# Optimization experiments

Hardware: AMD Instinct MI355X
Metric: run time of the kernel (lower is better)

The kernel has to match this reference:

```python
import jax, jax.numpy as jnp
import numpy as np

N, CIN, T, V, COUT = 64, 64, 256, 25, 128
CI = COUT // 2  # inter_channels
EPS = 1e-5


def setup_inputs() -> dict:
    key = jax.random.key(0)
    ks = jax.random.split(key, 12)
    s = 0.05
    d = {}
    d['x'] = jax.random.normal(ks[0], (N, CIN, T, V), jnp.float32)
    d['A'] = jax.random.normal(ks[1], (3, V, V), jnp.float32) * s
    d['Al'] = jax.random.normal(ks[2], (3, V, V), jnp.float32) * s
    d['Wp'] = jax.random.normal(ks[3], (3, COUT, CIN), jnp.float32) * s
    d['bp'] = jnp.zeros((3, COUT), jnp.float32)
    d['Wm1'] = jax.random.normal(ks[4], (CI, CIN), jnp.float32) * s
    d['bm1'] = jnp.zeros((CI,), jnp.float32)
    d['Wm2'] = jax.random.normal(ks[5], (CI, CIN), jnp.float32) * s
    d['bm2'] = jnp.zeros((CI,), jnp.float32)
    d['Wm3'] = jax.random.normal(ks[6], (COUT, CI), jnp.float32) * s
    d['bm3'] = jnp.zeros((COUT,), jnp.float32)
    d['Wm4'] = jax.random.normal(ks[7], (COUT, CIN), jnp.float32) * s
    d['bm4'] = jnp.zeros((COUT,), jnp.float32)
    d['alpha'] = jax.random.normal(ks[8], (1,), jnp.float32) * s
    d['bn_gamma'] = jnp.ones((COUT,), jnp.float32)
    d['bn_beta'] = jnp.zeros((COUT,), jnp.float32)
    d['down_W'] = jax.random.normal(ks[9], (COUT, CIN), jnp.float32) * s
    d['down_gamma'] = jnp.ones((COUT,), jnp.float32)
    d['down_beta'] = jnp.zeros((COUT,), jnp.float32)
    return d


def _bn_train(y, gamma, beta):
    # BatchNorm2d training forward: biased batch stats over (N, T, V)
    mu = jnp.mean(y, axis=(0, 2, 3), keepdims=True)
    var = jnp.var(y, axis=(0, 2, 3), keepdims=True)
    return (y - mu) * jax.lax.rsqrt(var + EPS) * gamma[None, :, None, None] + beta[None, :, None, None]


def reference(x, A, Al, Wp, bp, Wm1, bm1, Wm2, bm2, Wm3, bm3, Wm4, bm4,
              alpha, bn_gamma, bn_beta, down_W, down_gamma, down_beta):
    Tn = x.shape[2]
    # --- static graph branch: sum over 3 subsets of (A+Al) graph matmuls ---
    Xp = jnp.einsum('soi,nitv->snotv', Wp, x) + bp[:, None, :, None, None]  # (3,N,COUT,T,V)
    y = jnp.einsum('suv,snctv->nctu', A + Al, Xp)                           # (N,COUT,T,V)
    # --- dynamic adjacency from temporal-difference features ---
    xf = jnp.mean(jnp.einsum('oi,nitv->notv', Wm1, x[:, :, :Tn - 2]) + bm1[None, :, None, None], axis=2)  # (N,CI,V)
    xb = jnp.mean(jnp.einsum('oi,nitv->notv', Wm2, x[:, :, 2:]) + bm2[None, :, None, None], axis=2)       # (N,CI,V)
    diff = xb[:, :, :, None] - xf[:, :, None, :]                            # (N,CI,V,V)
    Rd = jnp.tanh(jnp.einsum('oi,nivw->novw', Wm3, diff) + bm3[None, :, None, None])  # (N,COUT,V,V)
    Xm = jnp.einsum('oi,nitv->notv', Wm4, x) + bm4[None, :, None, None]     # (N,COUT,T,V)
    z = jnp.einsum('ncuv,nctv->nctu', Rd, Xm)                               # (N,COUT,T,V)
    y = z * alpha + y
    # --- BN, residual (1x1 conv + BN down-path since CIN != COUT), ReLU ---
    y = _bn_train(y, bn_gamma, bn_beta)
    d = jnp.einsum('oi,nitv->notv', down_W, x)  # no bias
    d = _bn_train(d, down_gamma, down_beta)
    return jax.nn.relu(y + d)
```

## Files before the change

### kernel.cpp

```cpp
#include <hip/hip_runtime.h>
#include <stdint.h>

typedef unsigned short u16;
typedef unsigned int   u32;
typedef short bf16x8 __attribute__((ext_vector_type(8)));
typedef float f32x4  __attribute__((ext_vector_type(4)));

#define N_    64
#define CIN_  64
#define T_    256
#define V_    25
#define COUT_ 128
#define CI_   64
#define EPS_  1e-5f
#define CNT_  409600.0f

#define MFMA16(a,b,c) __builtin_amdgcn_mfma_f32_16x16x32_bf16((a),(b),(c),0,0,0)

__device__ __forceinline__ u16 f2bf(float f) {
  u32 u = __float_as_uint(f);
  u += 0x7fffu + ((u >> 16) & 1u);
  return (u16)(u >> 16);
}
__device__ __forceinline__ float bf2f(u16 h) { return __uint_as_float(((u32)h) << 16); }

__global__ __launch_bounds__(256) void k_pack(const float* __restrict__ Wp, const float* __restrict__ Wm4,
                                              const float* __restrict__ dW, const float* __restrict__ A,
                                              const float* __restrict__ Al,
                                              u16* __restrict__ w5, u16* __restrict__ bst) {
  int tid = threadIdx.x;
  for (int i = tid; i < 640 * 64; i += 256) {
    int r = i >> 6, k = i & 63;
    float v = (r < 384) ? Wp[i] : (r < 512) ? Wm4[(r - 384) * 64 + k] : dW[(r - 512) * 64 + k];
    w5[i] = f2bf(v);
  }
  for (int i = tid; i < 3 * 32 * 32; i += 256) {
    int s = i >> 10, rem = i & 1023, u = rem >> 5, v = rem & 31;
    float val = (u < 25 && v < 25) ? (A[(s * 25 + u) * 25 + v] + Al[(s * 25 + u) * 25 + v]) : 0.f;
    bst[i] = f2bf(val);
  }
}

__global__ __launch_bounds__(256) void k_means(const float* __restrict__ x,
                                               float* __restrict__ mf, float* __restrict__ mb) {
  int i = blockIdx.x, n = blockIdx.y;
  const float* src = x + ((size_t)n * CIN_ + i) * T_ * V_;
  __shared__ float xs[T_ * V_];
  __shared__ float pf[8][32], pb[8][32];
  for (int idx = threadIdx.x; idx < T_ * V_; idx += 256) xs[idx] = src[idx];
  __syncthreads();
  int v = threadIdx.x & 31, g = threadIdx.x >> 5;
  float sf = 0.f, sb = 0.f;
  if (v < V_) {
    for (int t = g; t < T_; t += 8) {
      float val = xs[t * V_ + v];
      if (t < T_ - 2) sf += val;
      if (t >= 2)     sb += val;
    }
  }
  pf[g][v] = sf; pb[g][v] = sb;
  __syncthreads();
  if (threadIdx.x < V_) {
    float af = 0.f, ab = 0.f;
    for (int gg = 0; gg < 8; gg++) { af += pf[gg][threadIdx.x]; ab += pb[gg][threadIdx.x]; }
    size_t o = ((size_t)n * CIN_ + i) * V_ + threadIdx.x;
    mf[o] = af * (1.0f / 254.0f);
    mb[o] = ab * (1.0f / 254.0f);
  }
}

__global__ __launch_bounds__(256) void k_rd(
    const float* __restrict__ mf, const float* __restrict__ mb,
    const float* __restrict__ Wm1, const float* __restrict__ bm1,
    const float* __restrict__ Wm2, const float* __restrict__ bm2,
    const float* __restrict__ Wm3, const float* __restrict__ bm3,
    const float* __restrict__ bm4, const float* __restrict__ alpha,
    const float* __restrict__ A, const float* __restrict__ Al, const float* __restrict__ bp,
    u16* __restrict__ rdws, float* __restrict__ biasws) {
  int n = blockIdx.x;
  int tid = threadIdx.x;
  __shared__ float MfL[CIN_][V_], MbL[CIN_][V_], xfL[CI_][V_], xbL[CI_][V_];
  __shared__ float PL[COUT_ * V_], QL[COUT_ * V_], rsumL[3][V_];
  for (int idx = tid; idx < CIN_ * V_; idx += 256) {
    MfL[idx / V_][idx % V_] = mf[(size_t)n * CIN_ * V_ + idx];
    MbL[idx / V_][idx % V_] = mb[(size_t)n * CIN_ * V_ + idx];
  }
  if (tid < 75) {
    int s = tid / 25, u = tid % 25;
    float acc = 0.f;
    for (int v = 0; v < 25; v++) acc += A[(s * 25 + u) * 25 + v] + Al[(s * 25 + u) * 25 + v];
    rsumL[s][u] = acc;
  }
  __syncthreads();
  for (int idx = tid; idx < CI_ * V_; idx += 256) {
    int o = idx / V_, v = idx % V_;
    float af = bm1[o], ab = bm2[o];
    for (int i = 0; i < CIN_; i++) {
      af += Wm1[o * CIN_ + i] * MfL[i][v];
      ab += Wm2[o * CIN_ + i] * MbL[i][v];
    }
    xfL[o][v] = af; xbL[o][v] = ab;
  }
  __syncthreads();
  for (int idx = tid; idx < COUT_ * V_; idx += 256) {
    int c = idx / V_, u = idx % V_;
    float p = 0.f, q = 0.f;
    for (int i = 0; i < CI_; i++) {
      p += Wm3[c * CI_ + i] * xbL[i][u];
      q += Wm3[c * CI_ + i] * xfL[i][u];
    }
    PL[idx] = p; QL[idx] = q;
  }
  __syncthreads();
  float al = alpha[0];
  for (int r = tid; r < COUT_ * V_; r += 256) {
    int c = r / V_, u = r % V_;
    float pv = PL[r] + bm3[c];
    float acc = 0.f;
    u16* dst = rdws + ((size_t)(n * COUT_ + c) * 25 + u) * 32;
    for (int w = 0; w < 25; w++) {
      float val = al * tanhf(pv - QL[c * V_ + w]);
      dst[w] = f2bf(val);
      acc += val;
    }
    for (int w = 25; w < 32; w++) dst[w] = 0;
    float yb = 0.f;
    for (int s = 0; s < 3; s++) yb += bp[s * COUT_ + c] * rsumL[s][u];
    biasws[(size_t)(n * COUT_ + c) * 25 + u] = bm4[c] * acc + yb;
  }
}

__global__ __launch_bounds__(256, 2) void k_main(
    const float* __restrict__ x, const u16* __restrict__ w5, const u16* __restrict__ bst,
    const u16* __restrict__ rdws, const float* __restrict__ biasws,
    u16* __restrict__ out16, float* __restrict__ partials) {
  __shared__ __align__(16) char smem[59904];
  __shared__ float statsL[512];
  const int tid = threadIdx.x;
  const int w = tid >> 6, l = tid & 63;
  const int lc = l & 15, lq = l >> 4;
  const int n = blockIdx.y, tc = blockIdx.x, t0 = tc * 16;

  {
    u32* xslw = (u32*)smem;
    const float* xb = x + (size_t)n * CIN_ * T_ * V_ + (size_t)t0 * V_;
    for (int idx = tid; idx < 32 * 416; idx += 256) {
      int i2 = idx / 416, p = idx - i2 * 416;
      float a = 0.f, b = 0.f;
      if (p < 400) {
        a = xb[(size_t)(2 * i2)     * (T_ * V_) + p];
        b = xb[(size_t)(2 * i2 + 1) * (T_ * V_) + p];
      }
      xslw[p * 36 + i2] = ((u32)f2bf(b) << 16) | (u32)f2bf(a);
    }
  }
  bf16x8 bw[3][2];
  #pragma unroll
  for (int s = 0; s < 3; s++)
    #pragma unroll
    for (int ut = 0; ut < 2; ut++)
      bw[s][ut] = *(const bf16x8*)(bst + (s * 32 + ut * 16 + lc) * 32 + lq * 8);
  __syncthreads();

  bf16x8 xf[7][2] = {};
  #pragma unroll
  for (int pi = 0; pi < 7; pi++) {
    int pt = w + pi * 4;
    if (pt < 26) {
      #pragma unroll
      for (int ks = 0; ks < 2; ks++)
        xf[pi][ks] = *(const bf16x8*)((const u16*)smem + (pt * 16 + lc) * 72 + ks * 32 + lq * 8);
    }
  }
  __syncthreads();

  {
    uint4 z4 = {0, 0, 0, 0};
    uint4* q = (uint4*)smem;
    for (int idx = tid; idx < 2304; idx += 256) q[idx] = z4;
    statsL[tid] = 0.f; statsL[tid + 256] = 0.f;
  }
  __syncthreads();

  u16* xpl = (u16*)smem;
  const f32x4 zz = {0.f, 0.f, 0.f, 0.f};

  for (int g = 0; g < 8; g++) {
    const int c0 = g * 16;
    f32x4 acc[4][2];
    #pragma unroll
    for (int cl = 0; cl < 4; cl++) { acc[cl][0] = zz; acc[cl][1] = zz; }
    float ds[4] = {0.f, 0.f, 0.f, 0.f}, dq[4] = {0.f, 0.f, 0.f, 0.f};

    #pragma unroll
    for (int h = 0; h < 2; h++) {
      const int nsl = h ? 3 : 2;
      bf16x8 af[3][2];
      #pragma unroll
      for (int si = 0; si < 3; si++) if (si < nsl) {
        int sl = h * 2 + si;
        #pragma unroll
        for (int ks = 0; ks < 2; ks++)
          af[si][ks] = *(const bf16x8*)(w5 + ((sl * 128 + c0 + lc) * 64 + ks * 32 + lq * 8));
      }
      #pragma unroll
      for (int pi = 0; pi < 7; pi++) {
        int pt = w + pi * 4;
        if (pt >= 26) continue;
        f32x4 pa[3];
        #pragma unroll
        for (int si = 0; si < 3; si++) if (si < nsl) {
          pa[si] = MFMA16(af[si][0], xf[pi][0], zz);
          pa[si] = MFMA16(af[si][1], xf[pi][1], pa[si]);
        }
        int p = pt * 16 + lc;
        if (p < 400) {
          u32 up = (u32)p, t = up / 25u, v = up - t * 25u;
          #pragma unroll
          for (int si = 0; si < 3; si++) if (si < nsl) {
            int sl = h * 2 + si;
            if (sl < 4) {
              int slot = sl & 1;
              u16* dst = xpl + (4 * lq) * 1152 + t * 72 + slot * 32 + v;
              #pragma unroll
              for (int r = 0; r < 4; r++) dst[r * 1152] = f2bf(pa[si][r]);
            } else {
              size_t ob = (((size_t)(n * COUT_ + c0 + 4 * lq) * T_ + t0 + t) * V_ + v) * 2 + 1;
              #pragma unroll
              for (int r = 0; r < 4; r++) {
                float dv = pa[si][r];
                out16[ob + (size_t)r * (T_ * V_ * 2)] = f2bf(dv);
                ds[r] += dv; dq[r] += dv * dv;
              }
            }
          }
        }
      }
      if (h == 1) {
        #pragma unroll
        for (int r = 0; r < 4; r++) {
          float a = ds[r], b = dq[r];
          #pragma unroll
          for (int off = 1; off < 16; off <<= 1) { a += __shfl_xor(a, off); b += __shfl_xor(b, off); }
          if (lc == 0) {
            atomicAdd(&statsL[(c0 + 4 * lq + r) * 4 + 2], a);
            atomicAdd(&statsL[(c0 + 4 * lq + r) * 4 + 3], b);
          }
        }
      }
      __syncthreads();

      {
        bf16x8 rdf0[4], rdf1[4];
        if (h == 1) {
          #pragma unroll
          for (int cl = 0; cl < 4; cl++) {
            size_t rb = (size_t)(n * COUT_ + c0 + w * 4 + cl) * 25;
            rdf0[cl] = *(const bf16x8*)(rdws + (rb + lc) * 32 + lq * 8);
            int u1c = (lc + 16 < 25) ? lc + 16 : 24;
            rdf1[cl] = *(const bf16x8*)(rdws + (rb + u1c) * 32 + lq * 8);
          }
        }
        #pragma unroll
        for (int cl = 0; cl < 4; cl++) {
          int clocal = w * 4 + cl;
          #pragma unroll
          for (int kl = 0; kl < 2; kl++) {
            bf16x8 aX = *(const bf16x8*)(xpl + clocal * 1152 + lc * 72 + kl * 32 + lq * 8);
            int kk = h * 2 + kl;
            bf16x8 b0, b1;
            if (kk < 3) { b0 = bw[kk][0]; b1 = bw[kk][1]; }
            else        { b0 = rdf0[cl];  b1 = rdf1[cl]; }
            acc[cl][0] = MFMA16(aX, b0, acc[cl][0]);
            acc[cl][1] = MFMA16(aX, b1, acc[cl][1]);
          }
        }
      }
      if (h == 1) {
        #pragma unroll
        for (int cl = 0; cl < 4; cl++) {
          int c = c0 + w * 4 + cl;
          size_t bb = (size_t)(n * COUT_ + c) * 25;
          float bias0 = biasws[bb + lc];
          int u1 = lc + 16; bool v1 = u1 < 25;
          float bias1 = biasws[bb + (v1 ? u1 : 24)];
          size_t ob = ((size_t)(n * COUT_ + c) * T_ + t0) * V_;
          float sy = 0.f, sq = 0.f;
          #pragma unroll
          for (int r = 0; r < 4; r++) {
            int t = 4 * lq + r;
            float y0 = acc[cl][0][r] + bias0;
            out16[(ob + t * 25 + lc) * 2] = f2bf(y0);
            sy += y0; sq += y0 * y0;
            float y1 = acc[cl][1][r] + bias1;
            if (v1) {
              out16[(ob + t * 25 + u1) * 2] = f2bf(y1);
              sy += y1; sq += y1 * y1;
            }
          }
          #pragma unroll
          for (int off = 1; off < 64; off <<= 1) { sy += __shfl_xor(sy, off); sq += __shfl_xor(sq, off); }
          if (l == 0) { atomicAdd(&statsL[c * 4 + 0], sy); atomicAdd(&statsL[c * 4 + 1], sq); }
        }
      }
      __syncthreads();
    }
  }
  int bflat = blockIdx.y * 16 + blockIdx.x;
  for (int j = tid; j < 512; j += 256) partials[(size_t)j * 1024 + bflat] = statsL[j];
}

__global__ __launch_bounds__(256) void k_stats1(const float* __restrict__ partials, float* __restrict__ colsum) {
  int w = threadIdx.x >> 6, l = threadIdx.x & 63;
  for (int ci = 0; ci < 8; ci++) {
    int j = blockIdx.x * 32 + w * 8 + ci;
    float s = 0.f;
    for (int it = 0; it < 16; it++) s += partials[(size_t)j * 1024 + it * 64 + l];
    #pragma unroll
    for (int off = 1; off < 64; off <<= 1) s += __shfl_xor(s, off);
    if (l == 0) colsum[j] = s;
  }
}

__global__ __launch_bounds__(128) void k_stats2(
    const float* __restrict__ colsum,
    const float* __restrict__ bn_g, const float* __restrict__ bn_b,
    const float* __restrict__ dn_g, const float* __restrict__ dn_b,
    float* __restrict__ params) {
  int c = threadIdx.x;
  float sy = colsum[c * 4], syy = colsum[c * 4 + 1], sd = colsum[c * 4 + 2], sdd = colsum[c * 4 + 3];
  float muY = sy / CNT_, varY = syy / CNT_ - muY * muY;
  float muD = sd / CNT_, varD = sdd / CNT_ - muD * muD;
  float sY = bn_g[c] * rsqrtf(varY + EPS_);
  float sD = dn_g[c] * rsqrtf(varD + EPS_);
  float off = bn_b[c] - muY * sY + dn_b[c] - muD * sD;
  params[c * 4 + 0] = sY; params[c * 4 + 1] = sD; params[c * 4 + 2] = off;
}

__global__ __launch_bounds__(256) void k_final(u32* __restrict__ io, const float* __restrict__ params) {
  int slab = blockIdx.x;
  int c = slab & (COUT_ - 1);
  float sY = params[c * 4], sD = params[c * 4 + 1], off = params[c * 4 + 2];
  size_t base = (size_t)slab * (T_ * V_);
  #pragma unroll 5
  for (int j = 0; j < 25; j++) {
    size_t idx = base + j * 256 + threadIdx.x;
    u32 w = io[idx];
    float y = bf2f((u16)(w & 0xffffu));
    float d = bf2f((u16)(w >> 16));
    float val = fmaf(y, sY, fmaf(d, sD, off));
    io[idx] = __float_as_uint(fmaxf(val, 0.0f));
  }
}

extern "C" void kernel_launch(void* const* d_in, const int* in_sizes, int n_in,
                              void* d_out, int out_size, void* d_ws, size_t ws_size,
                              hipStream_t stream) {
  const float* x    = (const float*)d_in[0];
  const float* A    = (const float*)d_in[1];
  const float* Al   = (const float*)d_in[2];
  const float* Wp   = (const float*)d_in[3];
  const float* bp   = (const float*)d_in[4];
  const float* Wm1  = (const float*)d_in[5];
  const float* bm1  = (const float*)d_in[6];
  const float* Wm2  = (const float*)d_in[7];
  const float* bm2  = (const float*)d_in[8];
  const float* Wm3  = (const float*)d_in[9];
  const float* bm3  = (const float*)d_in[10];
  const float* Wm4  = (const float*)d_in[11];
  const float* bm4  = (const float*)d_in[12];
  const float* alpha= (const float*)d_in[13];
  const float* bn_g = (const float*)d_in[14];
  const float* bn_b = (const float*)d_in[15];
  const float* dW   = (const float*)d_in[16];
  const float* dn_g = (const float*)d_in[17];
  const float* dn_b = (const float*)d_in[18];

  char* ws = (char*)d_ws;
  float* mf       = (float*)(ws + 0);
  float* mb       = (float*)(ws + 409600);
  u16*   rdws     = (u16*)  (ws + 819200);
  float* biasws   = (float*)(ws + 13926400);
  u16*   w5       = (u16*)  (ws + 14745600);
  u16*   bstw     = (u16*)  (ws + 14827520);
  float* partials = (float*)(ws + 14833664);
  float* colsum   = (float*)(ws + 16930816);
  float* params   = (float*)(ws + 16932864);

  k_pack <<<dim3(1),       dim3(256), 0, stream>>>(Wp, Wm4, dW, A, Al, w5, bstw);
  k_means<<<dim3(64, 64),  dim3(256), 0, stream>>>(x, mf, mb);
  k_rd   <<<dim3(64),      dim3(256), 0, stream>>>(mf, mb, Wm1, bm1, Wm2, bm2, Wm3, bm3,
                                                   bm4, alpha, A, Al, bp, rdws, biasws);
  k_main <<<dim3(16, 64),  dim3(256), 0, stream>>>(x, w5, bstw, rdws, biasws,
                                                   (u16*)d_out, partials);
  k_stats1<<<dim3(16),     dim3(256), 0, stream>>>(partials, colsum);
  k_stats2<<<dim3(1),      dim3(128), 0, stream>>>(colsum, bn_g, bn_b, dn_g, dn_b, params);
  k_final<<<dim3(64 * 128),dim3(256), 0, stream>>>((u32*)d_out, params);
}
```

Baseline: 679.5 us.

## Shrink k_main LDS for 3 blocks/CU, stage down-path in LDS, vectorize final pass

k_main now stages x in two 32-channel halves, which cuts shared memory so the launch bounds can ask for three blocks per CU instead of two. The down-path conv output is buffered in LDS and written with y as one packed 32-bit store, replacing scattered 16-bit global stores. Its statistics are reduced in the same epilogue pass as y. Separately, k_pack and k_stats1 get wider grids and k_final uses 128-bit loads and stores. The risk is register pressure under the tighter occupancy target and the extra LDS traffic and barriers.

```diff
diff --git a/kernel.cpp b/kernel.cpp
--- a/kernel.cpp
+++ b/kernel.cpp
@@ -28,13 +28,13 @@
                                               const float* __restrict__ dW, const float* __restrict__ A,
                                               const float* __restrict__ Al,
                                               u16* __restrict__ w5, u16* __restrict__ bst) {
-  int tid = threadIdx.x;
-  for (int i = tid; i < 640 * 64; i += 256) {
+  int tid0 = blockIdx.x * 256 + threadIdx.x, stride = gridDim.x * 256;
+  for (int i = tid0; i < 640 * 64; i += stride) {
     int r = i >> 6, k = i & 63;
     float v = (r < 384) ? Wp[i] : (r < 512) ? Wm4[(r - 384) * 64 + k] : dW[(r - 512) * 64 + k];
     w5[i] = f2bf(v);
   }
-  for (int i = tid; i < 3 * 32 * 32; i += 256) {
+  for (int i = tid0; i < 3 * 32 * 32; i += stride) {
     int s = i >> 10, rem = i & 1023, u = rem >> 5, v = rem & 31;
     float val = (u < 25 && v < 25) ? (A[(s * 25 + u) * 25 + v] + Al[(s * 25 + u) * 25 + v]) : 0.f;
     bst[i] = f2bf(val);
@@ -130,29 +130,37 @@
   }
 }
 
-__global__ __launch_bounds__(256, 2) void k_main(
+__global__ __launch_bounds__(256, 3) void k_main(
     const float* __restrict__ x, const u16* __restrict__ w5, const u16* __restrict__ bst,
     const u16* __restrict__ rdws, const float* __restrict__ biasws,
-    u16* __restrict__ out16, float* __restrict__ partials) {
-  __shared__ __align__(16) char smem[59904];
+    u32* __restrict__ out32, float* __restrict__ partials) {
+  __shared__ __align__(16) char smem[36864];
+  __shared__ u16 dls[16 * 425];
   __shared__ float statsL[512];
   const int tid = threadIdx.x;
   const int w = tid >> 6, l = tid & 63;
   const int lc = l & 15, lq = l >> 4;
   const int n = blockIdx.y, tc = blockIdx.x, t0 = tc * 16;
 
-  {
+  bf16x8 xf[7][2] = {};
+  const float* xb = x + (size_t)n * CIN_ * T_ * V_ + (size_t)t0 * V_;
+  #pragma unroll
+  for (int hf = 0; hf < 2; hf++) {
     u32* xslw = (u32*)smem;
-    const float* xb = x + (size_t)n * CIN_ * T_ * V_ + (size_t)t0 * V_;
-    for (int idx = tid; idx < 32 * 416; idx += 256) {
-      int i2 = idx / 416, p = idx - i2 * 416;
-      float a = 0.f, b = 0.f;
-      if (p < 400) {
-        a = xb[(size_t)(2 * i2)     * (T_ * V_) + p];
-        b = xb[(size_t)(2 * i2 + 1) * (T_ * V_) + p];
-      }
-      xslw[p * 36 + i2] = ((u32)f2bf(b) << 16) | (u32)f2bf(a);
-    }
+    for (int idx = tid; idx < 16 * 400; idx += 256) {
+      int i2 = idx / 400, p = idx - i2 * 400;
+      float a = xb[(size_t)(hf * 32 + 2 * i2)     * (T_ * V_) + p];
+      float b = xb[(size_t)(hf * 32 + 2 * i2 + 1) * (T_ * V_) + p];
+      xslw[p * 18 + i2] = ((u32)f2bf(b) << 16) | (u32)f2bf(a);
+    }
+    __syncthreads();
+    #pragma unroll
+    for (int pi = 0; pi < 7; pi++) {
+      int pt = w + pi * 4;
+      if (pt < 25)
+        xf[pi][hf] = *(const bf16x8*)((const u16*)smem + (pt * 16 + lc) * 36 + lq * 8);
+    }
+    __syncthreads();
   }
   bf16x8 bw[3][2];
   #pragma unroll
@@ -160,19 +168,6 @@
     #pragma unroll
     for (int ut = 0; ut < 2; ut++)
       bw[s][ut] = *(const bf16x8*)(bst + (s * 32 + ut * 16 + lc) * 32 + lq * 8);
-  __syncthreads();
-
-  bf16x8 xf[7][2] = {};
-  #pragma unroll
-  for (int pi = 0; pi < 7; pi++) {
-    int pt = w + pi * 4;
-    if (pt < 26) {
-      #pragma unroll
-      for (int ks = 0; ks < 2; ks++)
-        xf[pi][ks] = *(const bf16x8*)((const u16*)smem + (pt * 16 + lc) * 72 + ks * 32 + lq * 8);
-    }
-  }
-  __syncthreads();
 
   {
     uint4 z4 = {0, 0, 0, 0};
@@ -190,7 +185,6 @@
     f32x4 acc[4][2];
     #pragma unroll
     for (int cl = 0; cl < 4; cl++) { acc[cl][0] = zz; acc[cl][1] = zz; }
-    float ds[4] = {0.f, 0.f, 0.f, 0.f}, dq[4] = {0.f, 0.f, 0.f, 0.f};
 
     #pragma unroll
     for (int h = 0; h < 2; h++) {
@@ -206,101 +200,88 @@
       #pragma unroll
       for (int pi = 0; pi < 7; pi++) {
         int pt = w + pi * 4;
-        if (pt >= 26) continue;
+        if (pt >= 25) continue;
         f32x4 pa[3];
         #pragma unroll
         for (int si = 0; si < 3; si++) if (si < nsl) {
           pa[si] = MFMA16(af[si][0], xf[pi][0], zz);
           pa[si] = MFMA16(af[si][1], xf[pi][1], pa[si]);
         }
-        int p = pt * 16 + lc;
-        if (p < 400) {
-          u32 up = (u32)p, t = up / 25u, v = up - t * 25u;
-          #pragma unroll
-          for (int si = 0; si < 3; si++) if (si < nsl) {
-            int sl = h * 2 + si;
-            if (sl < 4) {
-              int slot = sl & 1;
-              u16* dst = xpl + (4 * lq) * 1152 + t * 72 + slot * 32 + v;
-              #pragma unroll
-              for (int r = 0; r < 4; r++) dst[r * 1152] = f2bf(pa[si][r]);
-            } else {
-              size_t ob = (((size_t)(n * COUT_ + c0 + 4 * lq) * T_ + t0 + t) * V_ + v) * 2 + 1;
-              #pragma unroll
-              for (int r = 0; r < 4; r++) {
-                float dv = pa[si][r];
-                out16[ob + (size_t)r * (T_ * V_ * 2)] = f2bf(dv);
-                ds[r] += dv; dq[r] += dv * dv;
-              }
-            }
+        u32 up = (u32)(pt * 16 + lc), t = up / 25u, v = up - t * 25u;
+        #pragma unroll
+        for (int si = 0; si < 3; si++) if (si < nsl) {
+          int sl = h * 2 + si;
+          if (sl < 4) {
+            int slot = sl & 1;
+            u16* dst = xpl + (4 * lq) * 1152 + t * 72 + slot * 32 + v;
+            #pragma unroll
+            for (int r = 0; r < 4; r++) dst[r * 1152] = f2bf(pa[si][r]);
+          } else {
+            u16* dst = dls + (4 * lq) * 425 + t * 26 + v;
+            #pragma unroll
+            for (int r = 0; r < 4; r++) dst[r * 425] = f2bf(pa[si][r]);
           }
         }
       }
+      __syncthreads();
+
+      bf16x8 rdf0[4], rdf1[4];
       if (h == 1) {
         #pragma unroll
-        for (int r = 0; r < 4; r++) {
-          float a = ds[r], b = dq[r];
-          #pragma unroll
-          for (int off = 1; off < 16; off <<= 1) { a += __shfl_xor(a, off); b += __shfl_xor(b, off); }
-          if (lc == 0) {
-            atomicAdd(&statsL[(c0 + 4 * lq + r) * 4 + 2], a);
-            atomicAdd(&statsL[(c0 + 4 * lq + r) * 4 + 3], b);
-          }
-        }
-      }
-      __syncthreads();
-
-      {
-        bf16x8 rdf0[4], rdf1[4];
-        if (h == 1) {
-          #pragma unroll
-          for (int cl = 0; cl < 4; cl++) {
-            size_t rb = (size_t)(n * COUT_ + c0 + w * 4 + cl) * 25;
-            rdf0[cl] = *(const bf16x8*)(rdws + (rb + lc) * 32 + lq * 8);
-            int u1c = (lc + 16 < 25) ? lc + 16 : 24;
-            rdf1[cl] = *(const bf16x8*)(rdws + (rb + u1c) * 32 + lq * 8);
-          }
-        }
-        #pragma unroll
         for (int cl = 0; cl < 4; cl++) {
-          int clocal = w * 4 + cl;
-          #pragma unroll
-          for (int kl = 0; kl < 2; kl++) {
-            bf16x8 aX = *(const bf16x8*)(xpl + clocal * 1152 + lc * 72 + kl * 32 + lq * 8);
-            int kk = h * 2 + kl;
-            bf16x8 b0, b1;
-            if (kk < 3) { b0 = bw[kk][0]; b1 = bw[kk][1]; }
-            else        { b0 = rdf0[cl];  b1 = rdf1[cl]; }
-            acc[cl][0] = MFMA16(aX, b0, acc[cl][0]);
-            acc[cl][1] = MFMA16(aX, b1, acc[cl][1]);
-          }
+          size_t rb = (size_t)(n * COUT_ + c0 + w * 4 + cl) * 25;
+          rdf0[cl] = *(const bf16x8*)(rdws + (rb + lc) * 32 + lq * 8);
+          int u1c = (lc + 16 < 25) ? lc + 16 : 24;
+          rdf1[cl] = *(const bf16x8*)(rdws + (rb + u1c) * 32 + lq * 8);
+        }
+      }
+      #pragma unroll
+      for (int cl = 0; cl < 4; cl++) {
+        int clocal = w * 4 + cl;
+        #pragma unroll
+        for (int kl = 0; kl < 2; kl++) {
+          bf16x8 aX = *(const bf16x8*)(xpl + clocal * 1152 + lc * 72 + kl * 32 + lq * 8);
+          int kk = h * 2 + kl;
+          bf16x8 b0, b1;
+          if (kk < 3) { b0 = bw[kk][0]; b1 = bw[kk][1]; }
+          else        { b0 = rdf0[cl];  b1 = rdf1[cl]; }
+          acc[cl][0] = MFMA16(aX, b0, acc[cl][0]);
+          acc[cl][1] = MFMA16(aX, b1, acc[cl][1]);
         }
       }
       if (h == 1) {
         #pragma unroll
         for (int cl = 0; cl < 4; cl++) {
-          int c = c0 + w * 4 + cl;
+          int cloc = w * 4 + cl, c = c0 + cloc;
           size_t bb = (size_t)(n * COUT_ + c) * 25;
           float bias0 = biasws[bb + lc];
           int u1 = lc + 16; bool v1 = u1 < 25;
           float bias1 = biasws[bb + (v1 ? u1 : 24)];
           size_t ob = ((size_t)(n * COUT_ + c) * T_ + t0) * V_;
-          float sy = 0.f, sq = 0.f;
+          float sy = 0.f, sq = 0.f, sd = 0.f, sdq = 0.f;
           #pragma unroll
           for (int r = 0; r < 4; r++) {
             int t = 4 * lq + r;
             float y0 = acc[cl][0][r] + bias0;
-            out16[(ob + t * 25 + lc) * 2] = f2bf(y0);
-            sy += y0; sq += y0 * y0;
-            float y1 = acc[cl][1][r] + bias1;
+            float d0 = bf2f(dls[cloc * 425 + t * 26 + lc]);
+            out32[ob + t * 25 + lc] = ((u32)f2bf(d0) << 16) | (u32)f2bf(y0);
+            sy += y0; sq += y0 * y0; sd += d0; sdq += d0 * d0;
             if (v1) {
-              out16[(ob + t * 25 + u1) * 2] = f2bf(y1);
-              sy += y1; sq += y1 * y1;
+              float y1 = acc[cl][1][r] + bias1;
+              float d1 = bf2f(dls[cloc * 425 + t * 26 + u1]);
+              out32[ob + t * 25 + u1] = ((u32)f2bf(d1) << 16) | (u32)f2bf(y1);
+              sy += y1; sq += y1 * y1; sd += d1; sdq += d1 * d1;
             }
           }
           #pragma unroll
-          for (int off = 1; off < 64; off <<= 1) { sy += __shfl_xor(sy, off); sq += __shfl_xor(sq, off); }
-          if (l == 0) { atomicAdd(&statsL[c * 4 + 0], sy); atomicAdd(&statsL[c * 4 + 1], sq); }
+          for (int off = 1; off < 64; off <<= 1) {
+            sy += __shfl_xor(sy, off); sq += __shfl_xor(sq, off);
+            sd += __shfl_xor(sd, off); sdq += __shfl_xor(sdq, off);
+          }
+          if (l == 0) {
+            atomicAdd(&statsL[c * 4 + 0], sy);  atomicAdd(&statsL[c * 4 + 1], sq);
+            atomicAdd(&statsL[c * 4 + 2], sd);  atomicAdd(&statsL[c * 4 + 3], sdq);
+          }
         }
       }
       __syncthreads();
@@ -311,15 +292,16 @@
 }
 
 __global__ __launch_bounds__(256) void k_stats1(const float* __restrict__ partials, float* __restrict__ colsum) {
-  int w = threadIdx.x >> 6, l = threadIdx.x & 63;
-  for (int ci = 0; ci < 8; ci++) {
-    int j = blockIdx.x * 32 + w * 8 + ci;
-    float s = 0.f;
-    for (int it = 0; it < 16; it++) s += partials[(size_t)j * 1024 + it * 64 + l];
-    #pragma unroll
-    for (int off = 1; off < 64; off <<= 1) s += __shfl_xor(s, off);
-    if (l == 0) colsum[j] = s;
-  }
+  __shared__ float red[4];
+  int j = blockIdx.x, tid = threadIdx.x;
+  float s = 0.f;
+  #pragma unroll
+  for (int i = 0; i < 4; i++) s += partials[(size_t)j * 1024 + i * 256 + tid];
+  #pragma unroll
+  for (int off = 1; off < 64; off <<= 1) s += __shfl_xor(s, off);
+  if ((tid & 63) == 0) red[tid >> 6] = s;
+  __syncthreads();
+  if (tid == 0) colsum[j] = red[0] + red[1] + red[2] + red[3];
 }
 
 __global__ __launch_bounds__(128) void k_stats2(
@@ -337,19 +319,26 @@
   params[c * 4 + 0] = sY; params[c * 4 + 1] = sD; params[c * 4 + 2] = off;
 }
 
-__global__ __launch_bounds__(256) void k_final(u32* __restrict__ io, const float* __restrict__ params) {
+__global__ __launch_bounds__(256) void k_final(uint4* __restrict__ io, const float* __restrict__ params) {
   int slab = blockIdx.x;
   int c = slab & (COUT_ - 1);
   float sY = params[c * 4], sD = params[c * 4 + 1], off = params[c * 4 + 2];
-  size_t base = (size_t)slab * (T_ * V_);
-  #pragma unroll 5
-  for (int j = 0; j < 25; j++) {
-    size_t idx = base + j * 256 + threadIdx.x;
-    u32 w = io[idx];
-    float y = bf2f((u16)(w & 0xffffu));
-    float d = bf2f((u16)(w >> 16));
-    float val = fmaf(y, sY, fmaf(d, sD, off));
-    io[idx] = __float_as_uint(fmaxf(val, 0.0f));
+  size_t base = (size_t)slab * 1600;
+  #pragma unroll
+  for (int j = 0; j < 7; j++) {
+    int idx = j * 256 + threadIdx.x;
+    if (idx < 1600) {
+      uint4 wv = io[base + idx];
+      u32 ws[4] = {wv.x, wv.y, wv.z, wv.w};
+      #pragma unroll
+      for (int e = 0; e < 4; e++) {
+        float y = bf2f((u16)(ws[e] & 0xffffu));
+        float d = bf2f((u16)(ws[e] >> 16));
+        float val = fmaf(y, sY, fmaf(d, sD, off));
+        ws[e] = __float_as_uint(fmaxf(val, 0.0f));
+      }
+      io[base + idx] = make_uint4(ws[0], ws[1], ws[2], ws[3]);
+    }
   }
 }
 
@@ -387,13 +376,13 @@
   float* colsum   = (float*)(ws + 16930816);
   float* params   = (float*)(ws + 16932864);
 
-  k_pack <<<dim3(1),       dim3(256), 0, stream>>>(Wp, Wm4, dW, A, Al, w5, bstw);
+  k_pack <<<dim3(41),      dim3(256), 0, stream>>>(Wp, Wm4, dW, A, Al, w5, bstw);
   k_means<<<dim3(64, 64),  dim3(256), 0, stream>>>(x, mf, mb);
   k_rd   <<<dim3(64),      dim3(256), 0, stream>>>(mf, mb, Wm1, bm1, Wm2, bm2, Wm3, bm3,
                                                    bm4, alpha, A, Al, bp, rdws, biasws);
   k_main <<<dim3(16, 64),  dim3(256), 0, stream>>>(x, w5, bstw, rdws, biasws,
-                                                   (u16*)d_out, partials);
-  k_stats1<<<dim3(16),     dim3(256), 0, stream>>>(partials, colsum);
+                                                   (u32*)d_out, partials);
+  k_stats1<<<dim3(512),    dim3(256), 0, stream>>>(partials, colsum);
   k_stats2<<<dim3(1),      dim3(128), 0, stream>>>(colsum, bn_g, bn_b, dn_g, dn_b, params);
-  k_final<<<dim3(64 * 128),dim3(256), 0, stream>>>((u32*)d_out, params);
-}
+  k_final<<<dim3(64 * 128),dim3(256), 0, stream>>>((uint4*)d_out, params);
+}
```

New measurement: 796.1 us. 1.17x slower.
